# Kernel tuning notes

Measured on AMD Instinct MI355X. Metric: run time of the kernel, lower is better.

Reference implementation:

```python
import jax, jax.numpy as jnp
import numpy as np

B, S, D = 64, 4096, 256

def setup_inputs() -> dict:
    key = jax.random.key(0)
    k1, k2, k3 = jax.random.split(key, 3)
    aspect = jax.random.normal(k1, (B, 1, D), dtype=jnp.float32)
    memory = jax.random.normal(k2, (B, S, D), dtype=jnp.float32)
    lim = np.sqrt(6.0 / (2 * D + 1)).astype(np.float32)
    W = jax.random.uniform(k3, (2 * D, 1), dtype=jnp.float32, minval=-lim, maxval=lim)
    b = jnp.zeros((1,), dtype=jnp.float32)
    return {"aspect": aspect, "memory": memory, "W": W, "b": b}

def reference(aspect, memory, W, b):
    # aspect: (B,1,D), memory: (B,S,D), W: (2D,1), b: (1,)
    # Original concatenates [memory, repeated_aspect] along -1 then dots with W.
    # Equivalent (and avoids materializing the (B,S,2D) concat):
    # scores = memory @ W[:D] + aspect @ W[D:] + b
    Wm, Wa = W[:memory.shape[-1]], W[memory.shape[-1]:]
    gi = jnp.tanh(jnp.einsum('bsd,do->bso', memory, Wm)
                  + jnp.einsum('bud,do->buo', aspect, Wa)  # (B,1,1) broadcasts over S
                  + b)
    gi = jnp.sum(gi, axis=-1)            # (B,S)
    alfa = jax.nn.softmax(gi, axis=-1)   # softmax over memory steps
    out = jnp.einsum('bsd,bs->bd', memory, alfa)  # weighted pooling -> (B,D)
    return out
```

## Files before the change

### kernel.cpp

```cpp
#include <hip/hip_runtime.h>

#define B_  64
#define S_  4096
#define D_  256
#define NC  16
#define ROWS_PER_CHUNK (S_ / NC)
#define ROWS_PER_WAVE  (ROWS_PER_CHUNK / 4)

__global__ __launch_bounds__(256) void attmem_pass1(
    const float* __restrict__ aspect,
    const float* __restrict__ memory,
    const float* __restrict__ W,
    const float* __restrict__ bias,
    float* __restrict__ ws_o,
    float* __restrict__ ws_l)
{
    const int chunk = blockIdx.x;
    const int batch = blockIdx.y;
    const int tid   = threadIdx.x;
    const int wave  = tid >> 6;
    const int lane  = tid & 63;

    const float4 wm = ((const float4*)W)[lane];
    const float4 wa = ((const float4*)(W + D_))[lane];
    const float4 av = ((const float4*)(aspect + batch * D_))[lane];

    float a0 = av.x * wa.x + av.y * wa.y + av.z * wa.z + av.w * wa.w;
    #pragma unroll
    for (int off = 32; off >= 1; off >>= 1) a0 += __shfl_xor(a0, off, 64);
    a0 += bias[0];

    const float4* mem4 = (const float4*)(memory + (size_t)batch * S_ * D_);
    const int s0 = chunk * ROWS_PER_CHUNK + wave * ROWS_PER_WAVE;

    float  l = 0.f;
    float4 o = make_float4(0.f, 0.f, 0.f, 0.f);

    #pragma unroll 4
    for (int i = 0; i < ROWS_PER_WAVE; ++i) {
        const int s = s0 + i;
        const float4 x = mem4[(size_t)s * (D_ / 4) + lane];

        float d = x.x * wm.x + x.y * wm.y + x.z * wm.z + x.w * wm.w;
        #pragma unroll
        for (int off = 32; off >= 1; off >>= 1) d += __shfl_xor(d, off, 64);

        const float g  = d + a0;
        const float e2 = __expf(2.f * g);
        const float th = (e2 - 1.f) / (e2 + 1.f);
        const float p  = __expf(th);

        l   += p;
        o.x += p * x.x;  o.y += p * x.y;  o.z += p * x.z;  o.w += p * x.w;
    }

    __shared__ float lds_o[4 * D_];
    __shared__ float lds_l[4];
    ((float4*)lds_o)[wave * (D_ / 4) + lane] = o;
    if (lane == 0) lds_l[wave] = l;
    __syncthreads();

    const float osum = lds_o[tid] + lds_o[D_ + tid] +
                       lds_o[2 * D_ + tid] + lds_o[3 * D_ + tid];
    ws_o[((size_t)batch * NC + chunk) * D_ + tid] = osum;
    if (tid == 0)
        ws_l[batch * NC + chunk] = lds_l[0] + lds_l[1] + lds_l[2] + lds_l[3];
}

__global__ __launch_bounds__(256) void attmem_pass2(
    const float* __restrict__ ws_o,
    const float* __restrict__ ws_l,
    float* __restrict__ out)
{
    const int batch = blockIdx.x;
    const int d     = threadIdx.x;

    float lsum = 0.f;
    #pragma unroll
    for (int c = 0; c < NC; ++c) lsum += ws_l[batch * NC + c];

    float osum = 0.f;
    #pragma unroll
    for (int c = 0; c < NC; ++c)
        osum += ws_o[((size_t)batch * NC + c) * D_ + d];

    out[batch * D_ + d] = osum / lsum;
}

extern "C" void kernel_launch(void* const* d_in, const int* in_sizes, int n_in,
                              void* d_out, int out_size, void* d_ws, size_t ws_size,
                              hipStream_t stream) {
    const float* aspect = (const float*)d_in[0];
    const float* memory = (const float*)d_in[1];
    const float* W      = (const float*)d_in[2];
    const float* bias   = (const float*)d_in[3];

    float* ws_o = (float*)d_ws;
    float* ws_l = ws_o + (size_t)B_ * NC * D_;

    dim3 grid1(NC, B_);
    attmem_pass1<<<grid1, 256, 0, stream>>>(aspect, memory, W, bias, ws_o, ws_l);
    attmem_pass2<<<B_, 256, 0, stream>>>(ws_o, ws_l, (float*)d_out);
}
```

Baseline: 367.8 us.

## Process two rows per wave with half-wave reductions and double chunk count

Each wave now splits into two 32-lane halves, each handling a separate memory row with two float4 loads per lane. This shortens the cross-lane shuffle reduction from six steps to five and doubles the rows in flight per instruction. Chunks per batch go from 16 to 32, doubling the grid to raise occupancy and memory-level parallelism. The cost is a larger LDS footprint and more partial results for the second pass to combine.

Measured after the change: 361.1 us (median of 2 runs). About the same (-1.8%).

```diff
diff --git a/kernel.cpp b/kernel.cpp
--- a/kernel.cpp
+++ b/kernel.cpp
@@ -3,9 +3,10 @@
 #define B_  64
 #define S_  4096
 #define D_  256
-#define NC  16
+#define NC  32
 #define ROWS_PER_CHUNK (S_ / NC)
 #define ROWS_PER_WAVE  (ROWS_PER_CHUNK / 4)
+#define ITERS (ROWS_PER_WAVE / 2)
 
 __global__ __launch_bounds__(256) void attmem_pass1(
     const float* __restrict__ aspect,
@@ -20,51 +21,71 @@
     const int tid   = threadIdx.x;
     const int wave  = tid >> 6;
     const int lane  = tid & 63;
+    const int half  = lane >> 5;
+    const int hl    = lane & 31;
 
-    const float4 wm = ((const float4*)W)[lane];
-    const float4 wa = ((const float4*)(W + D_))[lane];
-    const float4 av = ((const float4*)(aspect + batch * D_))[lane];
+    const float4* W4 = (const float4*)W;
+    const float4 wm0 = W4[hl * 2 + 0], wm1 = W4[hl * 2 + 1];
+    const float4 wa0 = W4[64 + hl * 2 + 0], wa1 = W4[64 + hl * 2 + 1];
+    const float4* A4 = (const float4*)(aspect + batch * D_);
+    const float4 av0 = A4[hl * 2 + 0], av1 = A4[hl * 2 + 1];
 
-    float a0 = av.x * wa.x + av.y * wa.y + av.z * wa.z + av.w * wa.w;
+    float a0 = av0.x * wa0.x + av0.y * wa0.y + av0.z * wa0.z + av0.w * wa0.w
+             + av1.x * wa1.x + av1.y * wa1.y + av1.z * wa1.z + av1.w * wa1.w;
     #pragma unroll
-    for (int off = 32; off >= 1; off >>= 1) a0 += __shfl_xor(a0, off, 64);
+    for (int off = 16; off >= 1; off >>= 1) a0 += __shfl_xor(a0, off, 64);
     a0 += bias[0];
 
     const float4* mem4 = (const float4*)(memory + (size_t)batch * S_ * D_);
     const int s0 = chunk * ROWS_PER_CHUNK + wave * ROWS_PER_WAVE;
 
-    float  l = 0.f;
-    float4 o = make_float4(0.f, 0.f, 0.f, 0.f);
+    float  l  = 0.f;
+    float4 o0 = make_float4(0.f, 0.f, 0.f, 0.f);
+    float4 o1 = make_float4(0.f, 0.f, 0.f, 0.f);
 
-    #pragma unroll 4
-    for (int i = 0; i < ROWS_PER_WAVE; ++i) {
-        const int s = s0 + i;
-        const float4 x = mem4[(size_t)s * (D_ / 4) + lane];
+    #pragma unroll 2
+    for (int i = 0; i < ITERS; ++i) {
+        const int s = s0 + 2 * i + half;
+        const size_t base = (size_t)s * (D_ / 4) + hl * 2;
+        const float4 x0 = mem4[base + 0];
+        const float4 x1 = mem4[base + 1];
 
-        float d = x.x * wm.x + x.y * wm.y + x.z * wm.z + x.w * wm.w;
+        float d = x0.x * wm0.x + x0.y * wm0.y + x0.z * wm0.z + x0.w * wm0.w
+                + x1.x * wm1.x + x1.y * wm1.y + x1.z * wm1.z + x1.w * wm1.w;
         #pragma unroll
-        for (int off = 32; off >= 1; off >>= 1) d += __shfl_xor(d, off, 64);
+        for (int off = 16; off >= 1; off >>= 1) d += __shfl_xor(d, off, 64);
 
         const float g  = d + a0;
         const float e2 = __expf(2.f * g);
-        const float th = (e2 - 1.f) / (e2 + 1.f);
-        const float p  = __expf(th);
+        const float p  = __expf((e2 - 1.f) / (e2 + 1.f));
 
-        l   += p;
-        o.x += p * x.x;  o.y += p * x.y;  o.z += p * x.z;  o.w += p * x.w;
+        l    += p;
+        o0.x += p * x0.x; o0.y += p * x0.y; o0.z += p * x0.z; o0.w += p * x0.w;
+        o1.x += p * x1.x; o1.y += p * x1.y; o1.z += p * x1.z; o1.w += p * x1.w;
     }
 
-    __shared__ float lds_o[4 * D_];
-    __shared__ float lds_l[4];
-    ((float4*)lds_o)[wave * (D_ / 4) + lane] = o;
-    if (lane == 0) lds_l[wave] = l;
+    __shared__ float lds_o[4 * 64 * 8];
+    __shared__ float lds_l[8];
+    float4* lo = (float4*)&lds_o[(wave * 64 + lane) * 8];
+    lo[0] = o0;
+    lo[1] = o1;
+    if (hl == 0) lds_l[wave * 2 + half] = l;
     __syncthreads();
 
-    const float osum = lds_o[tid] + lds_o[D_ + tid] +
-                       lds_o[2 * D_ + tid] + lds_o[3 * D_ + tid];
+    float osum = 0.f;
+    #pragma unroll
+    for (int w = 0; w < 4; ++w)
+        #pragma unroll
+        for (int h = 0; h < 2; ++h)
+            osum += lds_o[(w * 64 + h * 32 + (tid >> 3)) * 8 + (tid & 7)];
     ws_o[((size_t)batch * NC + chunk) * D_ + tid] = osum;
-    if (tid == 0)
-        ws_l[batch * NC + chunk] = lds_l[0] + lds_l[1] + lds_l[2] + lds_l[3];
+
+    if (tid == 0) {
+        float ls = 0.f;
+        #pragma unroll
+        for (int k = 0; k < 8; ++k) ls += lds_l[k];
+        ws_l[batch * NC + chunk] = ls;
+    }
 }
 
 __global__ __launch_bounds__(256) void attmem_pass2(
```
